# Kernel tuning notes

Hardware: AMD Instinct MI355X
Metric: run time of the kernel (lower is better)

## Reference

```python
import jax, jax.numpy as jnp
import numpy as np

B, C, N = 4, 3, 1024
D = H = W = 32

def setup_inputs() -> dict:
    key = jax.random.key(0)
    k1, k2 = jax.random.split(key)
    xyz = jax.random.normal(k1, (B, C, N), dtype=jnp.float32)
    grid = jax.random.uniform(k2, (C, D, H, W), dtype=jnp.float32)
    s1 = jnp.ones((1,), dtype=jnp.float32)
    s2 = jnp.ones((1,), dtype=jnp.float32)
    return {"xyz": xyz, "grid": grid, "s1": s1, "s2": s2}

def reference(xyz, grid, s1, s2):
    # dist[b,d,h,w,n] = sum_c (xyz[b,c,n] - grid[c,d,h,w])^2
    x2 = jnp.sum(xyz * xyz, axis=1)            # (B, N)
    g2 = jnp.sum(grid * grid, axis=0)          # (D, H, W)
    xg = jnp.einsum('bcn,cdhw->bdhwn', xyz, grid)  # (B, D, H, W, N)
    dist = x2[:, None, None, None, :] + g2[None, :, :, :, None] - 2.0 * xg
    v = jnp.abs(s2[0]) * jnp.exp(-jnp.abs(s1[0]) * dist)   # (B, D, H, W, N)
    v = jax.nn.softmax(v, axis=4)
    p, _ = jax.lax.top_k(v, 2)                 # top-2 over last axis (N)
    return p[..., 0] - p[..., 1]               # (B, D, H, W) top-2 margin
```

## Files before the change

### kernel.cpp

```cpp
#include <hip/hip_runtime.h>
#include <math.h>


#define LOG2E 1.44269504088896340736f

__global__ __launch_bounds__(256, 8) void p2v_kernel(
    const float* __restrict__ xyz,
    const float* __restrict__ grid,
    const float* __restrict__ s1,
    const float* __restrict__ s2,
    float* __restrict__ out)
{
    __shared__ float4 A[1024];

    const int tid = threadIdx.x;
    const int b   = blockIdx.x >> 9;
    const int k   = blockIdx.x & 511;
    const int dhw = (k << 6) + (tid >> 2);
    const int c   = tid & 3;

    const float s1a = fabsf(s1[0]);
    const float s2a = fabsf(s2[0]);
    const float c1  = LOG2E * s1a;
    const float Ls2 = LOG2E * s2a;

    const float* xb = xyz + b * 3072;
    #pragma unroll
    for (int i = 0; i < 4; ++i) {
        const int n = tid + i * 256;
        const float x = xb[n], y = xb[1024 + n], z = xb[2048 + n];
        const float x2 = fmaf(x, x, fmaf(y, y, z * z));
        A[n] = make_float4(-c1 * x2, 2.f * c1 * x, 2.f * c1 * y, 2.f * c1 * z);
    }
    __syncthreads();

    const float g0 = grid[dhw];
    const float g1 = grid[32768 + dhw];
    const float g2 = grid[65536 + dhw];
    const float EC = LOG2E * s2a *
        __builtin_amdgcn_exp2f(-c1 * fmaf(g0, g0, fmaf(g1, g1, g2 * g2)));

    float t0E = -INFINITY, t1E = -INFINITY, t0O = -INFINITY, t1O = -INFINITY;
    float S0 = 0.f, S1 = 0.f;

    const float4* Ac = A + c;
    #pragma unroll 8
    for (int i = 0; i < 256; ++i) {
        const float4 a = Ac[i << 2];
        const float q = fmaf(g0, a.y, fmaf(g1, a.z, fmaf(g2, a.w, a.x)));
        if (i & 1) {
            t1O = __builtin_amdgcn_fmed3f(t0O, t1O, q);
            t0O = fmaxf(t0O, q);
        } else {
            t1E = __builtin_amdgcn_fmed3f(t0E, t1E, q);
            t0E = fmaxf(t0E, q);
        }
        const float w = __builtin_amdgcn_exp2f(
            fmaf(EC, __builtin_amdgcn_exp2f(q), -Ls2));
        if (i & 1) S1 += w; else S0 += w;
    }

    float t0 = fmaxf(t0E, t0O);
    float t1 = fmaxf(fminf(t0E, t0O), fmaxf(t1E, t1O));
    float S  = S0 + S1;

    #pragma unroll
    for (int m = 1; m <= 2; m <<= 1) {
        const float ot0 = __shfl_xor(t0, m);
        const float ot1 = __shfl_xor(t1, m);
        const float oS  = __shfl_xor(S, m);
        t1 = fmaxf(fminf(t0, ot0), fmaxf(t1, ot1));
        t0 = fmaxf(t0, ot0);
        S += oS;
    }

    if (c == 0) {
        const float u0 = __builtin_amdgcn_exp2f(t0);
        const float u1 = __builtin_amdgcn_exp2f(t1);
        const float w0 = __builtin_amdgcn_exp2f(fmaf(EC, u0, -Ls2));
        const float num = w0 * (1.f - __builtin_amdgcn_exp2f(EC * (u1 - u0)));
        out[b * 32768 + dhw] = num / S;
    }
}

extern "C" void kernel_launch(void* const* d_in, const int* in_sizes, int n_in,
                              void* d_out, int out_size, void* d_ws, size_t ws_size,
                              hipStream_t stream) {
    const float* xyz  = (const float*)d_in[0];
    const float* grid = (const float*)d_in[1];
    const float* s1   = (const float*)d_in[2];
    const float* s2   = (const float*)d_in[3];
    float* out        = (float*)d_out;
    hipLaunchKernelGGL(p2v_kernel, dim3(2048), dim3(256), 0, stream,
                       xyz, grid, s1, s2, out);
}
```

Baseline: 97.54 us.

## Replace inner exp with squared Taylor polynomial and packed-FP32 pair processing

```diff
diff --git a/kernel.cpp b/kernel.cpp
--- a/kernel.cpp
+++ b/kernel.cpp
@@ -3,15 +3,16 @@
 
 
 #define LOG2E 1.44269504088896340736f
+typedef float f2 __attribute__((ext_vector_type(2)));
 
-__global__ __launch_bounds__(256, 8) void p2v_kernel(
+__global__ __launch_bounds__(256, 4) void p2v_kernel(
     const float* __restrict__ xyz,
     const float* __restrict__ grid,
     const float* __restrict__ s1,
     const float* __restrict__ s2,
     float* __restrict__ out)
 {
-    __shared__ float4 A[1024];
+    __shared__ float4 T[1024];
 
     const int tid = threadIdx.x;
     const int b   = blockIdx.x >> 9;
@@ -22,64 +23,127 @@
     const float s1a = fabsf(s1[0]);
     const float s2a = fabsf(s2[0]);
     const float c1  = LOG2E * s1a;
-    const float Ls2 = LOG2E * s2a;
 
     const float* xb = xyz + b * 3072;
     #pragma unroll
-    for (int i = 0; i < 4; ++i) {
-        const int n = tid + i * 256;
-        const float x = xb[n], y = xb[1024 + n], z = xb[2048 + n];
-        const float x2 = fmaf(x, x, fmaf(y, y, z * z));
-        A[n] = make_float4(-c1 * x2, 2.f * c1 * x, 2.f * c1 * y, 2.f * c1 * z);
+    for (int sidx = 2 * tid; sidx < 2 * tid + 2; ++sidx) {
+        const int p = sidx >> 2, cc = sidx & 3;
+        const int n0 = 8 * p + cc, n1 = n0 + 4;
+        const float x0 = xb[n0], y0 = xb[1024 + n0], z0 = xb[2048 + n0];
+        const float x1 = xb[n1], y1 = xb[1024 + n1], z1 = xb[2048 + n1];
+        const float q0 = -c1 * fmaf(x0, x0, fmaf(y0, y0, z0 * z0));
+        const float q1 = -c1 * fmaf(x1, x1, fmaf(y1, y1, z1 * z1));
+        T[2 * sidx]     = make_float4(q0, q1, 2.f * c1 * x0, 2.f * c1 * x1);
+        T[2 * sidx + 1] = make_float4(2.f * c1 * y0, 2.f * c1 * y1,
+                                      2.f * c1 * z0, 2.f * c1 * z1);
     }
     __syncthreads();
 
     const float g0 = grid[dhw];
     const float g1 = grid[32768 + dhw];
     const float g2 = grid[65536 + dhw];
-    const float EC = LOG2E * s2a *
-        __builtin_amdgcn_exp2f(-c1 * fmaf(g0, g0, fmaf(g1, g1, g2 * g2)));
+    const float Ct = s2a * __builtin_amdgcn_exp2f(
+        -c1 * fmaf(g0, g0, fmaf(g1, g1, g2 * g2)));
 
-    float t0E = -INFINITY, t1E = -INFINITY, t0O = -INFINITY, t1O = -INFINITY;
-    float S0 = 0.f, S1 = 0.f;
+    const float r  = 0.5f * Ct;
+    const float k1 = r;
+    const float k2 = r * k1 * 0.5f;
+    const float k3 = r * k2 * (1.f / 3.f);
+    const float k4 = r * k3 * 0.25f;
+    const float k5 = r * k4 * 0.2f;
+    const float k6 = r * k5 * (1.f / 6.f);
+    const float k7 = r * k6 * (1.f / 7.f);
 
-    const float4* Ac = A + c;
-    #pragma unroll 8
-    for (int i = 0; i < 256; ++i) {
-        const float4 a = Ac[i << 2];
-        const float q = fmaf(g0, a.y, fmaf(g1, a.z, fmaf(g2, a.w, a.x)));
-        if (i & 1) {
-            t1O = __builtin_amdgcn_fmed3f(t0O, t1O, q);
-            t0O = fmaxf(t0O, q);
-        } else {
-            t1E = __builtin_amdgcn_fmed3f(t0E, t1E, q);
-            t0E = fmaxf(t0E, q);
+    const float4* Tc = T + 2 * c;
+    float t0s, t1s, S;
+
+    if (s2a <= 1.0f) {
+        const f2 g0v = {g0, g0}, g1v = {g1, g1}, g2v = {g2, g2};
+        const f2 k1v = {k1, k1}, k2v = {k2, k2}, k3v = {k3, k3}, k4v = {k4, k4};
+        const f2 k5v = {k5, k5}, k6v = {k6, k6}, k7v = {k7, k7};
+        const f2 onev = {1.f, 1.f};
+        f2 t0v = {-INFINITY, -INFINITY}, t1v = {-INFINITY, -INFINITY};
+        f2 Sv = {0.f, 0.f};
+
+        #pragma unroll 8
+        for (int p = 0; p < 128; ++p) {
+            const float4 r0 = Tc[8 * p];
+            const float4 r1 = Tc[8 * p + 1];
+            const f2 ax = {r0.x, r0.y}, ay = {r0.z, r0.w};
+            const f2 az = {r1.x, r1.y}, aw = {r1.z, r1.w};
+            const f2 q = __builtin_elementwise_fma(aw, g2v,
+                         __builtin_elementwise_fma(az, g1v,
+                         __builtin_elementwise_fma(ay, g0v, ax)));
+            const f2 m = __builtin_elementwise_min(q, t0v);
+            t1v = __builtin_elementwise_max(t1v, m);
+            t0v = __builtin_elementwise_max(t0v, q);
+            f2 u;
+            u.x = __builtin_amdgcn_exp2f(q.x);
+            u.y = __builtin_amdgcn_exp2f(q.y);
+            f2 P = __builtin_elementwise_fma(k7v, u, k6v);
+            P = __builtin_elementwise_fma(P, u, k5v);
+            P = __builtin_elementwise_fma(P, u, k4v);
+            P = __builtin_elementwise_fma(P, u, k3v);
+            P = __builtin_elementwise_fma(P, u, k2v);
+            P = __builtin_elementwise_fma(P, u, k1v);
+            P = __builtin_elementwise_fma(P, u, onev);
+            Sv = __builtin_elementwise_fma(P, P, Sv);
         }
-        const float w = __builtin_amdgcn_exp2f(
-            fmaf(EC, __builtin_amdgcn_exp2f(q), -Ls2));
-        if (i & 1) S1 += w; else S0 += w;
+        t0s = fmaxf(t0v.x, t0v.y);
+        t1s = fmaxf(fminf(t0v.x, t0v.y), fmaxf(t1v.x, t1v.y));
+        S   = Sv.x + Sv.y;
+    } else {
+        const float EC  = LOG2E * Ct;
+        const float Ls2 = LOG2E * s2a;
+        float t0E = -INFINITY, t1E = -INFINITY, t0O = -INFINITY, t1O = -INFINITY;
+        float S0 = 0.f, S1 = 0.f;
+        #pragma unroll 4
+        for (int p = 0; p < 128; ++p) {
+            const float4 r0 = Tc[8 * p];
+            const float4 r1 = Tc[8 * p + 1];
+            const float qe = fmaf(g2, r1.z, fmaf(g1, r1.x, fmaf(g0, r0.z, r0.x)));
+            const float qo = fmaf(g2, r1.w, fmaf(g1, r1.y, fmaf(g0, r0.w, r0.y)));
+            t1E = __builtin_amdgcn_fmed3f(t0E, t1E, qe); t0E = fmaxf(t0E, qe);
+            t1O = __builtin_amdgcn_fmed3f(t0O, t1O, qo); t0O = fmaxf(t0O, qo);
+            S0 += __builtin_amdgcn_exp2f(fmaf(EC, __builtin_amdgcn_exp2f(qe), -Ls2));
+            S1 += __builtin_amdgcn_exp2f(fmaf(EC, __builtin_amdgcn_exp2f(qo), -Ls2));
+        }
+        t0s = fmaxf(t0E, t0O);
+        t1s = fmaxf(fminf(t0E, t0O), fmaxf(t1E, t1O));
+        S   = S0 + S1;
     }
-
-    float t0 = fmaxf(t0E, t0O);
-    float t1 = fmaxf(fminf(t0E, t0O), fmaxf(t1E, t1O));
-    float S  = S0 + S1;
 
     #pragma unroll
     for (int m = 1; m <= 2; m <<= 1) {
-        const float ot0 = __shfl_xor(t0, m);
-        const float ot1 = __shfl_xor(t1, m);
+        const float ot0 = __shfl_xor(t0s, m);
+        const float ot1 = __shfl_xor(t1s, m);
         const float oS  = __shfl_xor(S, m);
-        t1 = fmaxf(fminf(t0, ot0), fmaxf(t1, ot1));
-        t0 = fmaxf(t0, ot0);
-        S += oS;
+        t1s = fmaxf(fminf(t0s, ot0), fmaxf(t1s, ot1));
+        t0s = fmaxf(t0s, ot0);
+        S  += oS;
     }
 
     if (c == 0) {
-        const float u0 = __builtin_amdgcn_exp2f(t0);
-        const float u1 = __builtin_amdgcn_exp2f(t1);
-        const float w0 = __builtin_amdgcn_exp2f(fmaf(EC, u0, -Ls2));
-        const float num = w0 * (1.f - __builtin_amdgcn_exp2f(EC * (u1 - u0)));
-        out[b * 32768 + dhw] = num / S;
+        float res;
+        if (s2a <= 1.0f) {
+            const float u0 = __builtin_amdgcn_exp2f(t0s);
+            const float u1 = __builtin_amdgcn_exp2f(t1s);
+            float P0 = fmaf(k7, u0, k6);
+            P0 = fmaf(P0, u0, k5); P0 = fmaf(P0, u0, k4); P0 = fmaf(P0, u0, k3);
+            P0 = fmaf(P0, u0, k2); P0 = fmaf(P0, u0, k1); P0 = fmaf(P0, u0, 1.f);
+            float P1 = fmaf(k7, u1, k6);
+            P1 = fmaf(P1, u1, k5); P1 = fmaf(P1, u1, k4); P1 = fmaf(P1, u1, k3);
+            P1 = fmaf(P1, u1, k2); P1 = fmaf(P1, u1, k1); P1 = fmaf(P1, u1, 1.f);
+            res = (P0 * P0 - P1 * P1) / S;
+        } else {
+            const float EC  = LOG2E * Ct;
+            const float Ls2 = LOG2E * s2a;
+            const float u0 = __builtin_amdgcn_exp2f(t0s);
+            const float u1 = __builtin_amdgcn_exp2f(t1s);
+            const float w0 = __builtin_amdgcn_exp2f(fmaf(EC, u0, -Ls2));
+            res = w0 * (1.f - __builtin_amdgcn_exp2f(EC * (u1 - u0))) / S;
+        }
+        out[b * 32768 + dhw] = res;
     }
 }
 
```

After: 101.8 us. +4.4%, slower.

## Register-resident point table, wave-wide DPP reduction, polynomial inner exponential

Applied to the files above, without the earlier changes.

```diff
diff --git a/kernel.cpp b/kernel.cpp
--- a/kernel.cpp
+++ b/kernel.cpp
@@ -3,8 +3,42 @@
 
 
 #define LOG2E 1.44269504088896340736f
+#define PC0 1.0000247f
+#define PC1 0.9987113f
+#define PC2 0.5099871f
+#define PC3 0.1399751f
+#define PC4 0.0695533f
 
-__global__ __launch_bounds__(256, 8) void p2v_kernel(
+template<int CTRL, int RM, int BM>
+__device__ __forceinline__ float dpp_f(float x, float id) {
+    return __int_as_float(__builtin_amdgcn_update_dpp(
+        __float_as_int(id), __float_as_int(x), CTRL, RM, BM, false));
+}
+
+__device__ __forceinline__ float rlane_f(float x, int l) {
+    return __int_as_float(__builtin_amdgcn_readlane(__float_as_int(x), l));
+}
+
+template<int CTRL, int RM, int BM>
+__device__ __forceinline__ void red_step(float& t0, float& t1, float& S) {
+    const float a0 = dpp_f<CTRL, RM, BM>(t0, -INFINITY);
+    const float a1 = dpp_f<CTRL, RM, BM>(t1, -INFINITY);
+    const float aS = dpp_f<CTRL, RM, BM>(S, 0.f);
+    t1 = fmaxf(fmaxf(t1, a1), fminf(t0, a0));
+    t0 = fmaxf(t0, a0);
+    S += aS;
+}
+
+__device__ __forceinline__ void red64(float& t0, float& t1, float& S) {
+    red_step<0x111, 0xF, 0xF>(t0, t1, S);
+    red_step<0x112, 0xF, 0xF>(t0, t1, S);
+    red_step<0x114, 0xF, 0xE>(t0, t1, S);
+    red_step<0x118, 0xF, 0xC>(t0, t1, S);
+    red_step<0x142, 0xA, 0xF>(t0, t1, S);
+    red_step<0x143, 0x8, 0xF>(t0, t1, S);
+}
+
+__global__ __launch_bounds__(256, 4) void p2v_kernel(
     const float* __restrict__ xyz,
     const float* __restrict__ grid,
     const float* __restrict__ s1,
@@ -13,16 +47,16 @@
 {
     __shared__ float4 A[1024];
 
-    const int tid = threadIdx.x;
-    const int b   = blockIdx.x >> 9;
-    const int k   = blockIdx.x & 511;
-    const int dhw = (k << 6) + (tid >> 2);
-    const int c   = tid & 3;
+    const int tid  = threadIdx.x;
+    const int lane = tid & 63;
+    const int wv   = tid >> 6;
+    const int b    = blockIdx.x >> 9;
+    const int k    = blockIdx.x & 511;
+    const int obase = (k << 6) + (wv << 4);
 
     const float s1a = fabsf(s1[0]);
     const float s2a = fabsf(s2[0]);
     const float c1  = LOG2E * s1a;
-    const float Ls2 = LOG2E * s2a;
 
     const float* xb = xyz + b * 3072;
     #pragma unroll
@@ -34,53 +68,95 @@
     }
     __syncthreads();
 
-    const float g0 = grid[dhw];
-    const float g1 = grid[32768 + dhw];
-    const float g2 = grid[65536 + dhw];
-    const float EC = LOG2E * s2a *
-        __builtin_amdgcn_exp2f(-c1 * fmaf(g0, g0, fmaf(g1, g1, g2 * g2)));
+    float4 tab[16];
+    #pragma unroll
+    for (int j = 0; j < 16; ++j) tab[j] = A[lane + (j << 6)];
 
-    float t0E = -INFINITY, t1E = -INFINITY, t0O = -INFINITY, t1O = -INFINITY;
-    float S0 = 0.f, S1 = 0.f;
+    const int gi = obase + (lane & 15);
+    const float gv0 = grid[gi];
+    const float gv1 = grid[32768 + gi];
+    const float gv2 = grid[65536 + gi];
 
-    const float4* Ac = A + c;
-    #pragma unroll 8
-    for (int i = 0; i < 256; ++i) {
-        const float4 a = Ac[i << 2];
-        const float q = fmaf(g0, a.y, fmaf(g1, a.z, fmaf(g2, a.w, a.x)));
-        if (i & 1) {
-            t1O = __builtin_amdgcn_fmed3f(t0O, t1O, q);
-            t0O = fmaxf(t0O, q);
+    const bool fast = (s2a <= 1.0f);
+    float res = 0.f;
+
+    for (int o = 0; o < 16; ++o) {
+        const float g0 = rlane_f(gv0, o);
+        const float g1 = rlane_f(gv1, o);
+        const float g2 = rlane_f(gv2, o);
+        const float Ct = s2a * __builtin_amdgcn_exp2f(
+            -c1 * fmaf(g0, g0, fmaf(g1, g1, g2 * g2)));
+
+        float t0E = -INFINITY, t1E = -INFINITY, t0O = -INFINITY, t1O = -INFINITY;
+        float S0 = 0.f, S1 = 0.f;
+        float val;
+
+        if (fast) {
+            const float Ct2 = Ct * Ct;
+            const float d1 = PC1 * Ct;
+            const float d2 = PC2 * Ct2;
+            const float d3 = PC3 * Ct2 * Ct;
+            const float d4 = PC4 * Ct2 * Ct2;
+            #pragma unroll
+            for (int j = 0; j < 16; ++j) {
+                const float4 a = tab[j];
+                const float q = fmaf(g0, a.y, fmaf(g1, a.z, fmaf(g2, a.w, a.x)));
+                if (j & 1) {
+                    t1O = __builtin_amdgcn_fmed3f(t0O, t1O, q); t0O = fmaxf(t0O, q);
+                } else {
+                    t1E = __builtin_amdgcn_fmed3f(t0E, t1E, q); t0E = fmaxf(t0E, q);
+                }
+                const float u = __builtin_amdgcn_exp2f(q);
+                float Q = fmaf(d4, u, d3);
+                Q = fmaf(Q, u, d2);
+                Q = fmaf(Q, u, d1);
+                if (j & 1) S1 = fmaf(Q, u, S1); else S0 = fmaf(Q, u, S0);
+            }
+            float t0 = fmaxf(t0E, t0O);
+            float t1 = fmaxf(fminf(t0E, t0O), fmaxf(t1E, t1O));
+            float S  = S0 + S1;
+            red64(t0, t1, S);
+            const float t0s = rlane_f(t0, 63);
+            const float t1s = rlane_f(t1, 63);
+            const float Ss  = rlane_f(S, 63);
+            const float u0 = __builtin_amdgcn_exp2f(t0s);
+            const float u1 = __builtin_amdgcn_exp2f(t1s);
+            float Q0 = fmaf(d4, u0, d3); Q0 = fmaf(Q0, u0, d2); Q0 = fmaf(Q0, u0, d1);
+            float Q1 = fmaf(d4, u1, d3); Q1 = fmaf(Q1, u1, d2); Q1 = fmaf(Q1, u1, d1);
+            val = (Q0 * u0 - Q1 * u1) / fmaf(1024.f, PC0, Ss);
         } else {
-            t1E = __builtin_amdgcn_fmed3f(t0E, t1E, q);
-            t0E = fmaxf(t0E, q);
+            const float EC  = LOG2E * Ct;
+            const float Ls2 = LOG2E * s2a;
+            #pragma unroll
+            for (int j = 0; j < 16; ++j) {
+                const float4 a = tab[j];
+                const float q = fmaf(g0, a.y, fmaf(g1, a.z, fmaf(g2, a.w, a.x)));
+                if (j & 1) {
+                    t1O = __builtin_amdgcn_fmed3f(t0O, t1O, q); t0O = fmaxf(t0O, q);
+                } else {
+                    t1E = __builtin_amdgcn_fmed3f(t0E, t1E, q); t0E = fmaxf(t0E, q);
+                }
+                const float w = __builtin_amdgcn_exp2f(
+                    fmaf(EC, __builtin_amdgcn_exp2f(q), -Ls2));
+                if (j & 1) S1 += w; else S0 += w;
+            }
+            float t0 = fmaxf(t0E, t0O);
+            float t1 = fmaxf(fminf(t0E, t0O), fmaxf(t1E, t1O));
+            float S  = S0 + S1;
+            red64(t0, t1, S);
+            const float t0s = rlane_f(t0, 63);
+            const float t1s = rlane_f(t1, 63);
+            const float Ss  = rlane_f(S, 63);
+            const float u0 = __builtin_amdgcn_exp2f(t0s);
+            const float u1 = __builtin_amdgcn_exp2f(t1s);
+            const float w0 = __builtin_amdgcn_exp2f(fmaf(EC, u0, -Ls2));
+            val = w0 * (1.f - __builtin_amdgcn_exp2f(EC * (u1 - u0))) / Ss;
         }
-        const float w = __builtin_amdgcn_exp2f(
-            fmaf(EC, __builtin_amdgcn_exp2f(q), -Ls2));
-        if (i & 1) S1 += w; else S0 += w;
+
+        res = (lane == o) ? val : res;
     }
 
-    float t0 = fmaxf(t0E, t0O);
-    float t1 = fmaxf(fminf(t0E, t0O), fmaxf(t1E, t1O));
-    float S  = S0 + S1;
-
-    #pragma unroll
-    for (int m = 1; m <= 2; m <<= 1) {
-        const float ot0 = __shfl_xor(t0, m);
-        const float ot1 = __shfl_xor(t1, m);
-        const float oS  = __shfl_xor(S, m);
-        t1 = fmaxf(fminf(t0, ot0), fmaxf(t1, ot1));
-        t0 = fmaxf(t0, ot0);
-        S += oS;
-    }
-
-    if (c == 0) {
-        const float u0 = __builtin_amdgcn_exp2f(t0);
-        const float u1 = __builtin_amdgcn_exp2f(t1);
-        const float w0 = __builtin_amdgcn_exp2f(fmaf(EC, u0, -Ls2));
-        const float num = w0 * (1.f - __builtin_amdgcn_exp2f(EC * (u1 - u0)));
-        out[b * 32768 + dhw] = num / S;
-    }
+    if (lane < 16) out[b * 32768 + obase + lane] = res;
 }
 
 extern "C" void kernel_launch(void* const* d_in, const int* in_sizes, int n_in,
```

New measurement: 113.2 us. 16.0% more time.
